# Kernel tuning notes

Hardware: AMD Instinct MI355X
Metric: run time of the kernel (lower is better)

The kernel has to match this reference:

```python
import jax, jax.numpy as jnp
import numpy as np

_SAMPLING_EPS = 1e-5


def setup_inputs() -> dict:
    key = jax.random.key(0)
    k1, k2, k3, k4, k5 = jax.random.split(key, 5)
    B, V = 128, 128000
    logits = jax.random.normal(k1, (B, V), dtype=jnp.float32)
    temperature = jax.random.uniform(k2, (B,), dtype=jnp.float32)
    top_k = jax.random.randint(k3, (B,), 0, 1024)
    top_p = jax.random.uniform(k4, (B,), dtype=jnp.float32)
    # uniform noise -> exponential via -log(u) inside reference (torch's q.exponential_())
    q = jnp.clip(jax.random.uniform(k5, (B, V), dtype=jnp.float32), 1e-10, 1.0)
    return {"logits": logits, "temperature": temperature, "top_k": top_k,
            "top_p": top_p, "q": q, "max_num_logprobs": 5}


def reference(logits, temperature, top_k, top_p, q, max_num_logprobs):
    B, V = logits.shape
    # apply_temperature: temp < eps treated as 1.0 (greedy rows untouched)
    temp = jnp.where(temperature < _SAMPLING_EPS, 1.0, temperature)
    logits = logits.astype(jnp.float32) / temp[:, None]

    # _apply_top_k_top_p: ascending sort over vocab
    idx = jnp.argsort(logits, axis=-1)                      # [B, V]
    ls = jnp.take_along_axis(logits, idx, axis=-1)          # sorted ascending
    k = jnp.clip(top_k.astype(jnp.int32), 1, V)
    thr = jnp.take_along_axis(ls, (V - k)[:, None], axis=-1)  # k-th largest value
    ls = jnp.where(ls < thr, -jnp.inf, ls)
    # top-p on the top-k-masked sorted logits
    ps = jax.nn.softmax(ls, axis=-1)
    cum = jnp.cumsum(ps, axis=-1)
    p_mask = cum <= (1.0 - top_p)[:, None]
    p_mask = p_mask.at[:, -1].set(False)
    ls = jnp.where(p_mask, -jnp.inf, ls)
    # scatter masked sorted logits back to original vocab positions
    rows = jnp.arange(B)[:, None]
    logits = jnp.zeros_like(logits).at[rows, idx].set(ls)

    # get_probs + sample
    probs = jax.nn.softmax(logits, axis=-1)
    e = -jnp.log(q)                                         # exponential noise
    greedy = jnp.argmax(probs, axis=-1)
    rand = jnp.argmax(probs / e, axis=-1)                   # Gumbel-max equivalent
    sampled = jnp.where(temperature < _SAMPLING_EPS, greedy, rand).astype(jnp.int32)

    # top-k logprobs
    logprobs = jax.nn.log_softmax(logits, axis=-1)
    topk_logprobs, topk_indices = jax.lax.top_k(logprobs, max_num_logprobs)
    return sampled, topk_logprobs, topk_indices.astype(jnp.int32)
```

## Files before the change

kernel.cpp:

```cpp
#include <hip/hip_runtime.h>
#include <math.h>
#include <float.h>

typedef unsigned long long u64;
typedef unsigned u32;

#define NT 1024
#define NW 16
#define NT1 256
#define NT4 256
#define SL 8
#define NB 8192
#define BSH 19
#define CAP 2048
#define TOPN 5
#define SCALE_D 17592186044416.0
#define NEG_BIG -3.0e38f

struct RowCtl { u32 kb; u32 cnt0; u32 pad[30]; };

__device__ __forceinline__ u32 key_of(float f){
  u32 u = __float_as_uint(f);
  return (u & 0x80000000u) ? ~u : (u | 0x80000000u);
}
__device__ __forceinline__ float key_to_float(u32 k){
  u32 u = (k & 0x80000000u) ? (k & 0x7FFFFFFFu) : ~k;
  return __uint_as_float(u);
}
__device__ __forceinline__ u64 quantMass(float l, float m){
  float ef = expf(l - m);
  return (u64)((double)ef * SCALE_D + 0.5);
}

struct Top5 { float v[TOPN]; int ix[TOPN]; };
__device__ __forceinline__ void t5_init(Top5& t){
  for (int j=0;j<TOPN;j++){ t.v[j] = -INFINITY; t.ix[j] = 0x7FFFFFFF; }
}
__device__ __forceinline__ void t5_insert(Top5& t, float nv, int ni){
  for (int j=0;j<TOPN;j++){
    if (nv > t.v[j] || (nv == t.v[j] && ni < t.ix[j])){
      for (int s=TOPN-1;s>j;s--){ t.v[s]=t.v[s-1]; t.ix[s]=t.ix[s-1]; }
      t.v[j]=nv; t.ix[j]=ni;
      return;
    }
  }
}

__device__ void scan_excl(u64* arr, int n, u64* wsum){
  const int tid = threadIdx.x, lane = tid & 63, w = tid >> 6;
  __syncthreads();
  const int chunk = (n + NT - 1) / NT;
  const int base = tid * chunk;
  u64 local = 0;
  for (int j=0;j<chunk;j++){ int i=base+j; if (i<n) local += arr[i]; }
  u64 inc = local;
  for (int off=1; off<64; off<<=1){
    u64 up = __shfl_up(inc, off, 64);
    if (lane >= off) inc += up;
  }
  if (lane == 63) wsum[w] = inc;
  __syncthreads();
  if (tid == 0){
    u64 acc = 0;
    for (int i=0;i<NW;i++){ u64 v = wsum[i]; wsum[i] = acc; acc += v; }
    arr[n] = acc;
  }
  __syncthreads();
  u64 run = wsum[w] + (inc - local);
  for (int j=0;j<chunk;j++){ int i=base+j; if (i<n){ u64 v=arr[i]; arr[i]=run; run += v; } }
  __syncthreads();
}

__device__ __forceinline__ void scan_select(u64 (*h)[256], u64 targetIn, bool mkBudget,
        float pB, u32* o_bin, u64* o_excl, u64* o_T, u64* o_budget, int lane){
  const int base = lane*4;
  u64 c0 = h[0][base+0]+h[1][base+0]+h[2][base+0]+h[3][base+0];
  u64 c1 = h[0][base+1]+h[1][base+1]+h[2][base+1]+h[3][base+1];
  u64 c2 = h[0][base+2]+h[1][base+2]+h[2][base+2]+h[3][base+2];
  u64 c3 = h[0][base+3]+h[1][base+3]+h[2][base+3]+h[3][base+3];
  u64 lsum = c0+c1+c2+c3;
  u64 inc = lsum;
  for (int off=1; off<64; off<<=1){
    u64 up = __shfl_up(inc, off, 64);
    if (lane >= off) inc += up;
  }
  u64 total = __shfl(inc, 63, 64);
  u64 target = targetIn;
  if (mkBudget){
    float cf = 1.0f - pB;
    u64 q = (u64)((double)cf * (double)total);
    if (q >= total) q = total - 1;
    target = q;
    if (lane == 0){ *o_T = total; *o_budget = q; }
  }
  u64 run = inc - lsum;
  if (run<=target && target<run+c0){ *o_bin=(u32)base;   *o_excl=run; } run+=c0;
  if (run<=target && target<run+c1){ *o_bin=(u32)base+1; *o_excl=run; } run+=c1;
  if (run<=target && target<run+c2){ *o_bin=(u32)base+2; *o_excl=run; } run+=c2;
  if (run<=target && target<run+c3){ *o_bin=(u32)base+3; *o_excl=run; }
}


__global__ void k0_zero(u32* __restrict__ hist, u32* __restrict__ ctlw, int Bn){
  size_t n = (size_t)Bn * NB;
  size_t stride = (size_t)gridDim.x * blockDim.x;
  for (size_t i = (size_t)blockIdx.x*blockDim.x + threadIdx.x; i < n; i += stride) hist[i] = 0;
  size_t nc = (size_t)Bn * (sizeof(RowCtl)/4);
  for (size_t i = (size_t)blockIdx.x*blockDim.x + threadIdx.x; i < nc; i += stride) ctlw[i] = 0;
}

__global__ __launch_bounds__(NT1) void k1_hist(const float* __restrict__ L,
        const float* __restrict__ temp, u32* __restrict__ hist, int Bn, int Vn){
  __shared__ u32 lh[NB];
  const int b = blockIdx.y, s = blockIdx.x, tid = threadIdx.x;
  for (int j=tid;j<NB;j+=NT1) lh[j]=0;
  const float tr = temp[b]; const float tEff = (tr < 1e-5f) ? 1.0f : tr;
  const float* Lr = L + (size_t)b*Vn;
  const int chunk = (Vn + SL-1)/SL;
  const int i0 = s*chunk, i1 = min(i0+chunk, Vn);
  __syncthreads();
  const int nv = (i1 - i0) / 4;
  const float4* L4 = (const float4*)(Lr + i0);
  for (int v=tid; v<nv; v+=NT1){
    float4 x = L4[v];
    #pragma unroll
    for (int e=0;e<4;e++){
      float l = (&x.x)[e] / tEff;
      atomicAdd(&lh[key_of(l)>>BSH], 1u);
    }
  }
  for (int i=i0+nv*4+tid; i<i1; i+=NT1){
    float l = Lr[i]/tEff;
    atomicAdd(&lh[key_of(l)>>BSH], 1u);
  }
  __syncthreads();
  u32* Hr = hist + (size_t)b*NB;
  for (int j=tid;j<NB;j+=NT1){ u32 c = lh[j]; if (c) atomicAdd(&Hr[j], c); }
}

__global__ __launch_bounds__(NT) void k2_kb(const int* __restrict__ top_k,
        const u32* __restrict__ hist, RowCtl* __restrict__ ctl, int Bn, int Vn){
  __shared__ u32 sh[NB+1];
  __shared__ u32 wsum[NW];
  __shared__ int s_g;
  const int b = blockIdx.x, tid = threadIdx.x, lane = tid&63, w = tid>>6;
  const u32* Hr = hist + (size_t)b*NB;
  for (int j=tid;j<NB;j+=NT) sh[j] = Hr[j];
  __syncthreads();
  const int chunk = NB/NT;
  u32 local=0;
  for (int j=0;j<chunk;j++) local += sh[tid*chunk+j];
  u32 inc = local;
  for (int off=1;off<64;off<<=1){ u32 up=__shfl_up(inc,off,64); if (lane>=off) inc+=up; }
  if (lane==63) wsum[w]=inc;
  __syncthreads();
  if (tid==0){ u32 acc=0; for(int i=0;i<NW;i++){u32 v=wsum[i]; wsum[i]=acc; acc+=v;} sh[NB]=acc; }
  __syncthreads();
  u32 run = wsum[w] + (inc - local);
  for (int j=0;j<chunk;j++){ int i2=tid*chunk+j; u32 v=sh[i2]; sh[i2]=run; run+=v; }
  __syncthreads();
  int kk = top_k[b]; if (kk<1) kk=1; if (kk>Vn) kk=Vn;
  const u32 rank = (u32)(Vn - kk);
  for (int j=tid;j<NB;j+=NT) if (sh[j] <= rank && rank < sh[j+1]) s_g = j;
  __syncthreads();
  if (tid==0) ctl[b].kb = (u32)s_g;
}

__global__ __launch_bounds__(NT1) void k3_collect(const float* __restrict__ L,
        const float* __restrict__ temp, u64* __restrict__ cand, RowCtl* __restrict__ ctl,
        int Bn, int Vn){
  const int b = blockIdx.y, s = blockIdx.x, tid = threadIdx.x;
  const float tr = temp[b]; const float tEff = (tr<1e-5f)?1.0f:tr;
  const u32 kbMinKey = ctl[b].kb << BSH;
  const float* Lr = L + (size_t)b*Vn;
  u64* Cr = cand + (size_t)b*CAP;
  const int chunk = (Vn + SL-1)/SL;
  const int i0 = s*chunk, i1 = min(i0+chunk, Vn);
  const int nv = (i1 - i0) / 4;
  const float4* L4 = (const float4*)(Lr + i0);
  const int lane = tid & 63;
  for (int v=tid; v<nv; v+=NT1){
    float4 x = L4[v];
    #pragma unroll
    for (int e=0;e<4;e++){
      float l = (&x.x)[e] / tEff;
      u32 k = key_of(l);
      bool pred = (k >= kbMinKey);
      u64 mk = __ballot(pred);
      if (mk){
        int leader = __ffsll((long long)mk) - 1;
        u32 base = 0;
        if (lane == leader) base = atomicAdd(&ctl[b].cnt0, (u32)__popcll(mk));
        base = __shfl(base, leader, 64);
        if (pred){
          u32 p = base + (u32)__popcll(mk & ((1ull<<lane)-1ull));
          if (p < CAP) Cr[p] = ((u64)k<<32) | (u64)(u32)(i0 + v*4 + e);
        }
      }
    }
  }
  for (int i=i0+nv*4+tid; i<i1; i+=NT1){
    float l = Lr[i]/tEff;
    u32 k = key_of(l);
    if (k >= kbMinKey){
      u32 p = atomicAdd(&ctl[b].cnt0, 1u);
      if (p < CAP) Cr[p] = ((u64)k<<32) | (u64)(u32)i;
    }
  }
}

__global__ __launch_bounds__(NT4) void k4_solve(const float* __restrict__ L,
        const float* __restrict__ temp, const int* __restrict__ top_k,
        const float* __restrict__ top_p, const float* __restrict__ qn,
        const u64* __restrict__ cand, const RowCtl* __restrict__ ctl,
        float* __restrict__ out, int Bn, int Vn){
  __shared__ u32 sk[CAP];
  __shared__ u32 si[CAP];
  __shared__ u64 sm_[CAP];
  __shared__ u64 h[4][256];
  __shared__ u32 s_mk;
  __shared__ u32 s_bin;
  __shared__ u64 s_excl;
  __shared__ u64 s_T;
  __shared__ u64 s_budget;
  __shared__ float s_fill[16];
  __shared__ Top5 s_wt5[NT4/64];
  __shared__ double s_wr[NT4/64];
  __shared__ int s_wri[NT4/64];
  __shared__ int s_wg[NT4/64];

  const int b = blockIdx.x, tid = threadIdx.x, lane = tid&63, w = tid>>6;
  const u32 n0raw = ctl[b].cnt0;
  if (n0raw == 0 || n0raw > CAP) return;
  const int n0 = (int)n0raw;
  const float tr = temp[b]; const float tEff = (tr<1e-5f)?1.0f:tr;
  const float* Lr = L + (size_t)b*Vn;
  const float* Qr = qn + (size_t)b*Vn;
  const u64* Cr = cand + (size_t)b*CAP;

  if (tid==0) s_mk = 0;
  __syncthreads();
  u32 mk = 0;
  for (int p=tid; p<n0; p+=NT4){
    u64 e = Cr[p];
    u32 k = (u32)(e>>32);
    sk[p] = k; si[p] = (u32)e;
    mk = max(mk, k);
  }
  for (int off=32; off; off>>=1){ u32 o = __shfl_xor(mk, off, 64); mk = max(mk, o); }
  if (lane==0) atomicMax(&s_mk, mk);
  if (tid<16) s_fill[tid] = (tid<Vn) ? Lr[tid] : 0.f;
  __syncthreads();
  const u32 mKey = s_mk;
  const float m = key_to_float(mKey);

  int kk = top_k[b]; if (kk<1) kk=1; if (kk>Vn) kk=Vn; if (kk>n0) kk=n0;
  u64 rA = (u64)(n0 - kk);
  u32 pfx=0, pmask=0;
  for (int lev=0; lev<4; lev++){
    const int sh = 24 - 8*lev;
    for (int j=tid;j<1024;j+=NT4) ((u64*)h)[j] = 0;
    __syncthreads();
    for (int p=tid;p<n0;p+=NT4){
      u32 k = sk[p];
      if ((k & pmask) == pfx) atomicAdd(&h[w][(k>>sh)&0xFFu], 1ull);
    }
    __syncthreads();
    if (w==0) scan_select(h, rA, false, 0.f, &s_bin, &s_excl, 0, 0, lane);
    __syncthreads();
    pfx |= (s_bin << sh); pmask |= (0xFFu << sh);
    rA -= s_excl;
  }
  const u32 thrKey = pfx;

  for (int p=tid;p<n0;p+=NT4)
    sm_[p] = (sk[p] >= thrKey) ? quantMass(key_to_float(sk[p]), m) : 0ull;
  const float pB = top_p[b];

  u32 pfx2=0, pmask2=0;
  u64 Qloc=0, maskedBelow=0;
  for (int lev=0; lev<4; lev++){
    const int sh = 24 - 8*lev;
    for (int j=tid;j<1024;j+=NT4) ((u64*)h)[j] = 0;
    __syncthreads();
    for (int p=tid;p<n0;p+=NT4){
      u64 ms = sm_[p];
      if (ms && ((sk[p] & pmask2) == pfx2)) atomicAdd(&h[w][(sk[p]>>sh)&0xFFu], ms);
    }
    __syncthreads();
    if (w==0) scan_select(h, Qloc, lev==0, pB, &s_bin, &s_excl, &s_T, &s_budget, lane);
    __syncthreads();
    if (lev==0) Qloc = s_budget;
    pfx2 |= (s_bin << sh); pmask2 |= (0xFFu << sh);
    maskedBelow += s_excl;
    Qloc -= s_excl;
  }
  const u32 vKey = pfx2;
  const u64 T = s_T;
  const u64 qstar = quantMass(key_to_float(vKey), m);
  u64 tmask = qstar ? (Qloc / qstar) : 0ull;

  int idxStar = -1;
  if (tmask > 0){
    u64 r2 = tmask - 1;
    u32 ipfx=0, imask=0;
    for (int lev=0; lev<4; lev++){
      const int sh = 24 - 8*lev;
      for (int j=tid;j<1024;j+=NT4) ((u64*)h)[j] = 0;
      __syncthreads();
      for (int p=tid;p<n0;p+=NT4){
        if (sk[p]==vKey && ((si[p] & imask) == ipfx))
          atomicAdd(&h[w][(si[p]>>sh)&0xFFu], 1ull);
      }
      __syncthreads();
      if (w==0) scan_select(h, r2, false, 0.f, &s_bin, &s_excl, 0, 0, lane);
      __syncthreads();
      ipfx |= (s_bin << sh); imask |= (0xFFu << sh);
      r2 -= s_excl;
    }
    idxStar = (int)ipfx;
  }
  const u64 S2 = T - maskedBelow - tmask*qstar;

  Top5 t5; t5_init(t5);
  double br = -1.0; int bri = 0x7FFFFFFF; int gmin = 0x7FFFFFFF;
  for (int p=tid; p<n0; p+=NT4){
    u32 k = sk[p]; int idx = (int)si[p];
    bool surv = (k > vKey) || (k == vKey && idx > idxStar);
    if (surv){
      float l = key_to_float(k);
      float u = expf(l - m);
      float e = -logf(Qr[idx]);
      double ratio = (double)u / (double)e;
      if (ratio > br || (ratio == br && idx < bri)){ br = ratio; bri = idx; }
      if (k == mKey && idx < gmin) gmin = idx;
      t5_insert(t5, l, idx);
    }
  }
  for (int off=1; off<64; off<<=1){
    Top5 o;
    for (int j=0;j<TOPN;j++){ o.v[j]=__shfl_xor(t5.v[j],off,64); o.ix[j]=__shfl_xor(t5.ix[j],off,64); }
    for (int j=0;j<TOPN;j++) t5_insert(t5, o.v[j], o.ix[j]);
    double orr = __shfl_xor(br, off, 64); int ori = __shfl_xor(bri, off, 64);
    if (orr > br || (orr == br && ori < bri)){ br = orr; bri = ori; }
    int og = __shfl_xor(gmin, off, 64); if (og < gmin) gmin = og;
  }
  if (lane==0){ s_wt5[w]=t5; s_wr[w]=br; s_wri[w]=bri; s_wg[w]=gmin; }
  __syncthreads();
  if (tid==0){
    Top5 f = s_wt5[0];
    double fr = s_wr[0]; int fri = s_wri[0]; int fg = s_wg[0];
    for (int wi=1; wi<NT4/64; wi++){
      for (int j=0;j<TOPN;j++) t5_insert(f, s_wt5[wi].v[j], s_wt5[wi].ix[j]);
      if (s_wr[wi] > fr || (s_wr[wi]==fr && s_wri[wi]<fri)){ fr=s_wr[wi]; fri=s_wri[wi]; }
      if (s_wg[wi] < fg) fg = s_wg[wi];
    }
    int filled = 0;
    for (int i=0; i<16 && i<Vn && filled<TOPN; i++){
      u32 k2 = key_of(s_fill[i]/tEff);
      bool surv2 = (k2 > vKey) || (k2 == vKey && i > idxStar);
      if (!surv2){ t5_insert(f, -INFINITY, i); filled++; }
    }
    double lS = log((double)S2 / SCALE_D);
    int sampled = (tr < 1e-5f) ? fg : fri;
    out[b] = (float)sampled;
    for (int j=0;j<TOPN;j++){
      float lv = f.v[j];
      float lp = (lv == -INFINITY) ? NEG_BIG : (float)((double)lv - (double)m - lS);
      out[Bn + b*TOPN + j] = lp;
      out[Bn + Bn*TOPN + b*TOPN + j] = (float)f.ix[j];
    }
  }
}


__device__ void find_cross(const u64* arr, int n, u64 target, int* s_fh, u64* s_fb){
  const int tid = threadIdx.x;
  const int chunk = (n + NT - 1) / NT;
  const int base = tid * chunk;
  for (int j=0;j<chunk;j++){
    int i = base + j;
    if (i < n && arr[i] <= target && target < arr[i+1]){ *s_fh = i; *s_fb = arr[i]; }
  }
  __syncthreads();
}

__device__ void fallback_row(int b, const float* logits, const float* temperature,
                             const int* top_k, const float* top_p, const float* qnoise,
                             float* out, int Bn, int Vn){
  __shared__ u64 s_hist[4097];
  __shared__ u64 s_wsum[NW];
  __shared__ int s_fh;
  __shared__ u64 s_fb;
  __shared__ float s_fm[NW];
  __shared__ float s_m;
  __shared__ int s_lastMax;
  __shared__ int s_eqcnt;
  __shared__ int s_eqlist[1024];
  __shared__ int s_sel;
  __shared__ Top5 s_wt5[NW];
  __shared__ double s_wr[NW];
  __shared__ int s_wri[NW];
  __shared__ int s_wg[NW];
  __shared__ u64 s_ws2[NW];

  const int tid = threadIdx.x, lane = tid & 63, w = tid >> 6;
  const float* L  = logits + (size_t)b * Vn;
  const float* Qr = qnoise + (size_t)b * Vn;
  const float tRaw = temperature[b];
  const float tEff = (tRaw < 1e-5f) ? 1.0f : tRaw;

  for (int i=tid;i<4097;i+=NT) s_hist[i] = 0;
  if (tid==0){ s_lastMax = -1; s_eqcnt = 0; }
  __syncthreads();
  float lm = -INFINITY;
  for (int i=tid;i<Vn;i+=NT){
    float l = L[i] / tEff;
    u32 k = key_of(l);
    atomicAdd(&s_hist[k>>20], 1ull);
    lm = fmaxf(lm, l);
  }
  for (int off=32; off; off>>=1) lm = fmaxf(lm, __shfl_xor(lm, off, 64));
  if (lane==0) s_fm[w] = lm;
  scan_excl(s_hist, 4096, s_wsum);
  if (tid==0){ float mm=-INFINITY; for (int i=0;i<NW;i++) mm=fmaxf(mm,s_fm[i]); s_m=mm; }
  __syncthreads();
  const float m = s_m;

  int kk = top_k[b]; if (kk < 1) kk = 1; if (kk > Vn) kk = Vn;
  u64 r = (u64)(Vn - kk);
  find_cross(s_hist, 4096, r, &s_fh, &s_fb);
  const int kb0 = s_fh; r -= s_fb;
  __syncthreads();

  for (int i=tid;i<4097;i+=NT) s_hist[i]=0;
  __syncthreads();
  for (int i=tid;i<Vn;i+=NT){
    float l = L[i]/tEff; u32 k = key_of(l);
    if ((int)(k>>20) == kb0) atomicAdd(&s_hist[(k>>8)&0xFFFu], 1ull);
  }
  scan_excl(s_hist, 4096, s_wsum);
  find_cross(s_hist, 4096, r, &s_fh, &s_fb);
  const int kb1 = s_fh; r -= s_fb;
  __syncthreads();

  const u32 ktop24 = ((u32)kb0<<12) | (u32)kb1;
  for (int i=tid;i<4097;i+=NT) s_hist[i]=0;
  __syncthreads();
  for (int i=tid;i<Vn;i+=NT){
    float l = L[i]/tEff; u32 k = key_of(l);
    if ((k>>8) == ktop24) atomicAdd(&s_hist[k & 0xFFu], 1ull);
  }
  scan_excl(s_hist, 256, s_wsum);
  find_cross(s_hist, 256, r, &s_fh, &s_fb);
  const u32 thrKey = (ktop24<<8) | (u32)s_fh;
  const float thr = key_to_float(thrKey);
  __syncthreads();

  for (int i=tid;i<4097;i+=NT) s_hist[i]=0;
  __syncthreads();
  for (int i=tid;i<Vn;i+=NT){
    float l = L[i]/tEff;
    if (l >= thr){
      u32 k = key_of(l);
      double sd = exp((double)l - (double)m);
      u64 qv = (u64)(sd * SCALE_D + 0.5);
      atomicAdd(&s_hist[k>>20], qv);
      if (l == m) atomicMax(&s_lastMax, i);
    }
  }
  scan_excl(s_hist, 4096, s_wsum);
  const u64 T = s_hist[4096];
  const float cf = 1.0f - top_p[b];
  const double qtd = (double)cf * (double)T;
  u64 Qfix = (qtd >= (double)T) ? T : (u64)qtd;
  const bool allmask = (Qfix >= T);

  u32 vKey = 0xFFFFFFFFu;
  int idxStar = 0x7FFFFFFF;

  if (!allmask){
    find_cross(s_hist, 4096, Qfix, &s_fh, &s_fb);
    const int g0 = s_fh;
    u64 Qrem = Qfix - s_fb;
    __syncthreads();

    for (int i=tid;i<4097;i+=NT) s_hist[i]=0;
    __syncthreads();
    for (int i=tid;i<Vn;i+=NT){
      float l = L[i]/tEff;
      if (l >= thr){
        u32 k = key_of(l);
        if ((int)(k>>20) == g0){
          double sd = exp((double)l - (double)m);
          atomicAdd(&s_hist[(k>>8)&0xFFFu], (u64)(sd*SCALE_D+0.5));
        }
      }
    }
    scan_excl(s_hist, 4096, s_wsum);
    find_cross(s_hist, 4096, Qrem, &s_fh, &s_fb);
    const int g1 = s_fh; Qrem -= s_fb;
    __syncthreads();

    const u32 ptop24 = ((u32)g0<<12)|(u32)g1;
    for (int i=tid;i<4097;i+=NT) s_hist[i]=0;
    __syncthreads();
    for (int i=tid;i<Vn;i+=NT){
      float l = L[i]/tEff;
      if (l >= thr){
        u32 k = key_of(l);
        if ((k>>8) == ptop24){
          double sd = exp((double)l - (double)m);
          atomicAdd(&s_hist[k & 0xFFu], (u64)(sd*SCALE_D+0.5));
        }
      }
    }
    scan_excl(s_hist, 256, s_wsum);
    find_cross(s_hist, 256, Qrem, &s_fh, &s_fb);
    const int g2 = s_fh;
    const u64 base2 = s_fb;
    const u64 nextPref = s_hist[g2+1];
    Qrem -= base2;
    vKey = (ptop24<<8) | (u32)g2;
    const float vStar = key_to_float(vKey);
    const double sv = exp((double)vStar - (double)m);
    const u64 qstar = (u64)(sv*SCALE_D+0.5);
    u64 nstar = (qstar > 0) ? (nextPref - base2) / qstar : 1ull;
    if (nstar < 1) nstar = 1;
    u64 tmask = (qstar > 0) ? (Qrem / qstar) : 0ull;
    if (tmask >= nstar) tmask = nstar - 1;
    idxStar = -1;
    __syncthreads();
    if (tmask >= 1){
      for (int i=tid;i<Vn;i+=NT){
        float l = L[i]/tEff;
        if (key_of(l) == vKey){
          int p = atomicAdd(&s_eqcnt, 1);
          if (p < 1024) s_eqlist[p] = i;
        }
      }
      __syncthreads();
      if (tid == 0){
        int n_ = s_eqcnt; if (n_ > 1024) n_ = 1024;
        for (int a=1;a<n_;a++){
          int key0 = s_eqlist[a]; int c2=a-1;
          while (c2>=0 && s_eqlist[c2]>key0){ s_eqlist[c2+1]=s_eqlist[c2]; c2--; }
          s_eqlist[c2+1]=key0;
        }
        int ti = (int)tmask - 1;
        if (ti >= n_) ti = n_-1;
        s_sel = s_eqlist[ti];
      }
      __syncthreads();
      idxStar = s_sel;
    }
  }

  const int lastMax = s_lastMax;
  Top5 t5; t5_init(t5);
  u64 s2 = 0;
  double br = -1.0; int bri = 0x7FFFFFFF;
  int gmin = 0x7FFFFFFF;
  for (int i=tid;i<Vn;i+=NT){
    float l = L[i]/tEff;
    u32 k = key_of(l);
    bool surv = (l >= thr) &&
                ((k > vKey) || (k == vKey && i > idxStar) || (i == lastMax));
    float val;
    if (surv){
      double sd = exp((double)l - (double)m);
      s2 += (u64)(sd*SCALE_D+0.5);
      float u = expf(l - m);
      float e = -logf(Qr[i]);
      double ratio = (double)u / (double)e;
      if (ratio > br || (ratio == br && i < bri)){ br = ratio; bri = i; }
      if (l == m && i < gmin) gmin = i;
      val = l;
    } else {
      val = -INFINITY;
    }
    t5_insert(t5, val, i);
  }
  for (int off=1; off<64; off<<=1){
    Top5 o;
    for (int j=0;j<TOPN;j++){ o.v[j]=__shfl_xor(t5.v[j],off,64); o.ix[j]=__shfl_xor(t5.ix[j],off,64); }
    for (int j=0;j<TOPN;j++) t5_insert(t5, o.v[j], o.ix[j]);
    double orr = __shfl_xor(br, off, 64);
    int ori = __shfl_xor(bri, off, 64);
    if (orr > br || (orr == br && ori < bri)){ br = orr; bri = ori; }
    int og = __shfl_xor(gmin, off, 64); if (og < gmin) gmin = og;
    s2 += __shfl_xor(s2, off, 64);
  }
  if (lane == 0){
    s_wt5[w] = t5; s_wr[w]=br; s_wri[w]=bri; s_wg[w]=gmin; s_ws2[w]=s2;
  }
  __syncthreads();
  if (tid == 0){
    Top5 f = s_wt5[0];
    double fr = s_wr[0]; int fri = s_wri[0]; int fg = s_wg[0];
    u64 fs2 = s_ws2[0];
    for (int wi=1; wi<NW; wi++){
      for (int j=0;j<TOPN;j++) t5_insert(f, s_wt5[wi].v[j], s_wt5[wi].ix[j]);
      if (s_wr[wi] > fr || (s_wr[wi]==fr && s_wri[wi]<fri)){ fr=s_wr[wi]; fri=s_wri[wi]; }
      if (s_wg[wi] < fg) fg = s_wg[wi];
      fs2 += s_ws2[wi];
    }
    double S2d = (double)fs2 / SCALE_D;
    double lS = log(S2d);
    int sampled = (tRaw < 1e-5f) ? fg : fri;
    out[b] = (float)sampled;
    for (int j=0;j<TOPN;j++){
      float lv = f.v[j];
      float lp = (lv == -INFINITY) ? NEG_BIG : (float)((double)lv - (double)m - lS);
      out[Bn + b*TOPN + j] = lp;
      out[Bn + Bn*TOPN + b*TOPN + j] = (float)f.ix[j];
    }
  }
}

__global__ __launch_bounds__(NT) void k5_rowfb(const float* __restrict__ logits,
        const float* __restrict__ temperature, const int* __restrict__ top_k,
        const float* __restrict__ top_p, const float* __restrict__ qnoise,
        const RowCtl* __restrict__ ctl, float* __restrict__ out, int Bn, int Vn){
  const int b = blockIdx.x;
  const u32 c = ctl[b].cnt0;
  if (c > 0 && c <= CAP) return;
  fallback_row(b, logits, temperature, top_k, top_p, qnoise, out, Bn, Vn);
}

extern "C" __global__ void __launch_bounds__(NT)
sampler_fallback(const float* __restrict__ logits, const float* __restrict__ temperature,
                 const int* __restrict__ top_k, const float* __restrict__ top_p,
                 const float* __restrict__ qnoise, float* __restrict__ out, int Bn, int Vn){
  fallback_row(blockIdx.x, logits, temperature, top_k, top_p, qnoise, out, Bn, Vn);
}


extern "C" void kernel_launch(void* const* d_in, const int* in_sizes, int n_in,
                              void* d_out, int out_size, void* d_ws, size_t ws_size,
                              hipStream_t stream)
{
  const float* logits      = (const float*)d_in[0];
  const float* temperature = (const float*)d_in[1];
  const int*   top_k       = (const int*)d_in[2];
  const float* top_p       = (const float*)d_in[3];
  const float* q           = (const float*)d_in[4];
  const int Bn = in_sizes[1];
  const int Vn = in_sizes[0] / Bn;

  const size_t offCand = (size_t)Bn * NB * 4;
  const size_t offCtl  = offCand + (size_t)Bn * CAP * 8;
  const size_t total   = offCtl + (size_t)Bn * sizeof(RowCtl);

  if (ws_size < total){
    sampler_fallback<<<dim3(Bn), dim3(NT), 0, stream>>>(
        logits, temperature, top_k, top_p, q, (float*)d_out, Bn, Vn);
    return;
  }

  char* wsb = (char*)d_ws;
  u32*    hist = (u32*)wsb;
  u64*    cand = (u64*)(wsb + offCand);
  RowCtl* ctl  = (RowCtl*)(wsb + offCtl);

  k0_zero   <<<dim3(512),     dim3(256), 0, stream>>>(hist, (u32*)ctl, Bn);
  k1_hist   <<<dim3(SL, Bn),  dim3(NT1), 0, stream>>>(logits, temperature, hist, Bn, Vn);
  k2_kb     <<<dim3(Bn),      dim3(NT),  0, stream>>>(top_k, hist, ctl, Bn, Vn);
  k3_collect<<<dim3(SL, Bn),  dim3(NT1), 0, stream>>>(logits, temperature, cand, ctl, Bn, Vn);
  k4_solve  <<<dim3(Bn),      dim3(NT4), 0, stream>>>(logits, temperature, top_k, top_p, q,
                                                      cand, ctl, (float*)d_out, Bn, Vn);
  k5_rowfb  <<<dim3(Bn),      dim3(NT),  0, stream>>>(logits, temperature, top_k, top_p, q,
                                                      ctl, (float*)d_out, Bn, Vn);
}
```

Measured before the change: 139.7 us.

## Replace radix-histogram selection in solve kernel with register-resident bitwise radix select

The solve kernel now keeps each thread's candidate keys and indices in registers (8 per thread) instead of shared-memory arrays. The three 4-pass, 8-bit shared histogram selections (top-k threshold, top-p mass cutoff, tie index) become bit-by-bit binary searches using wave reductions and a small double-buffered shared slot. Searches start at the highest bit where the candidate floor and the max key differ. This removes the histogram clears, shared atomics and scan passes, at the cost of one barrier per bit and more iterations overall.

```diff
diff --git a/kernel.cpp b/kernel.cpp
--- a/kernel.cpp
+++ b/kernel.cpp
@@ -9,6 +9,7 @@
 #define NW 16
 #define NT1 256
 #define NT4 256
+#define EPT 8
 #define SL 8
 #define NB 8192
 #define BSH 19
@@ -69,35 +70,6 @@
   u64 run = wsum[w] + (inc - local);
   for (int j=0;j<chunk;j++){ int i=base+j; if (i<n){ u64 v=arr[i]; arr[i]=run; run += v; } }
   __syncthreads();
-}
-
-__device__ __forceinline__ void scan_select(u64 (*h)[256], u64 targetIn, bool mkBudget,
-        float pB, u32* o_bin, u64* o_excl, u64* o_T, u64* o_budget, int lane){
-  const int base = lane*4;
-  u64 c0 = h[0][base+0]+h[1][base+0]+h[2][base+0]+h[3][base+0];
-  u64 c1 = h[0][base+1]+h[1][base+1]+h[2][base+1]+h[3][base+1];
-  u64 c2 = h[0][base+2]+h[1][base+2]+h[2][base+2]+h[3][base+2];
-  u64 c3 = h[0][base+3]+h[1][base+3]+h[2][base+3]+h[3][base+3];
-  u64 lsum = c0+c1+c2+c3;
-  u64 inc = lsum;
-  for (int off=1; off<64; off<<=1){
-    u64 up = __shfl_up(inc, off, 64);
-    if (lane >= off) inc += up;
-  }
-  u64 total = __shfl(inc, 63, 64);
-  u64 target = targetIn;
-  if (mkBudget){
-    float cf = 1.0f - pB;
-    u64 q = (u64)((double)cf * (double)total);
-    if (q >= total) q = total - 1;
-    target = q;
-    if (lane == 0){ *o_T = total; *o_budget = q; }
-  }
-  u64 run = inc - lsum;
-  if (run<=target && target<run+c0){ *o_bin=(u32)base;   *o_excl=run; } run+=c0;
-  if (run<=target && target<run+c1){ *o_bin=(u32)base+1; *o_excl=run; } run+=c1;
-  if (run<=target && target<run+c2){ *o_bin=(u32)base+2; *o_excl=run; } run+=c2;
-  if (run<=target && target<run+c3){ *o_bin=(u32)base+3; *o_excl=run; }
 }
 
 
@@ -214,15 +186,8 @@
         const float* __restrict__ top_p, const float* __restrict__ qn,
         const u64* __restrict__ cand, const RowCtl* __restrict__ ctl,
         float* __restrict__ out, int Bn, int Vn){
-  __shared__ u32 sk[CAP];
-  __shared__ u32 si[CAP];
-  __shared__ u64 sm_[CAP];
-  __shared__ u64 h[4][256];
+  __shared__ u64 s_red[2][4];
   __shared__ u32 s_mk;
-  __shared__ u32 s_bin;
-  __shared__ u64 s_excl;
-  __shared__ u64 s_T;
-  __shared__ u64 s_budget;
   __shared__ float s_fill[16];
   __shared__ Top5 s_wt5[NT4/64];
   __shared__ double s_wr[NT4/64];
@@ -237,103 +202,156 @@
   const float* Lr = L + (size_t)b*Vn;
   const float* Qr = qn + (size_t)b*Vn;
   const u64* Cr = cand + (size_t)b*CAP;
+  const u32 kbMinKey = ctl[b].kb << BSH;
 
   if (tid==0) s_mk = 0;
-  __syncthreads();
+  if (tid<16) s_fill[tid] = (tid<Vn) ? Lr[tid] : 0.f;
+  __syncthreads();
+  u32 k_[EPT], ix_[EPT];
+  u32 valid = 0;
   u32 mk = 0;
-  for (int p=tid; p<n0; p+=NT4){
-    u64 e = Cr[p];
-    u32 k = (u32)(e>>32);
-    sk[p] = k; si[p] = (u32)e;
-    mk = max(mk, k);
-  }
-  for (int off=32; off; off>>=1){ u32 o = __shfl_xor(mk, off, 64); mk = max(mk, o); }
+  #pragma unroll
+  for (int e=0;e<EPT;e++){
+    int p = tid + e*NT4;
+    if (p < n0){
+      u64 v = Cr[p];
+      k_[e] = (u32)(v>>32); ix_[e] = (u32)v;
+      valid |= 1u<<e;
+      mk = max(mk, k_[e]);
+    } else { k_[e]=0u; ix_[e]=0u; }
+  }
+  for (int off=32; off; off>>=1){ u32 o=__shfl_xor(mk,off,64); mk=max(mk,o); }
   if (lane==0) atomicMax(&s_mk, mk);
-  if (tid<16) s_fill[tid] = (tid<Vn) ? Lr[tid] : 0.f;
   __syncthreads();
   const u32 mKey = s_mk;
   const float m = key_to_float(mKey);
+  int buf = 0;
 
   int kk = top_k[b]; if (kk<1) kk=1; if (kk>Vn) kk=Vn; if (kk>n0) kk=n0;
-  u64 rA = (u64)(n0 - kk);
-  u32 pfx=0, pmask=0;
-  for (int lev=0; lev<4; lev++){
-    const int sh = 24 - 8*lev;
-    for (int j=tid;j<1024;j+=NT4) ((u64*)h)[j] = 0;
+  u32 rA = (u32)(n0 - kk);
+  const u32 xA = kbMinKey ^ mKey;
+  const int sbA = xA ? (31 - __clz(xA)) : -1;
+  u32 pfx = (sbA==31) ? 0u : (mKey & ((sbA>=0) ? ~((1u<<(sbA+1))-1u) : 0xFFFFFFFFu));
+  u32 aA = valid;
+  for (int bit=sbA; bit>=0; --bit){
+    u32 c0 = 0;
+    #pragma unroll
+    for (int e=0;e<EPT;e++)
+      c0 += ((aA>>e)&1u) & (((k_[e]>>bit)&1u)^1u);
+    for (int off=32; off; off>>=1) c0 += __shfl_xor(c0, off, 64);
+    if (lane==0) s_red[buf][w] = (u64)c0;
     __syncthreads();
-    for (int p=tid;p<n0;p+=NT4){
-      u32 k = sk[p];
-      if ((k & pmask) == pfx) atomicAdd(&h[w][(k>>sh)&0xFFu], 1ull);
-    }
+    u32 C0 = (u32)(s_red[buf][0]+s_red[buf][1]+s_red[buf][2]+s_red[buf][3]);
+    u32 chosen;
+    if (rA < C0) chosen = 0u;
+    else { rA -= C0; chosen = 1u; pfx |= (1u<<bit); }
+    u32 na = 0;
+    #pragma unroll
+    for (int e=0;e<EPT;e++)
+      na |= (((aA>>e)&1u) & ((((k_[e]>>bit)&1u)==chosen)?1u:0u)) << e;
+    aA = na;
+    buf ^= 1;
+  }
+  const u32 thrKey = pfx;
+
+  u64 ms_[EPT];
+  u32 aB = 0;
+  u64 locT = 0;
+  #pragma unroll
+  for (int e=0;e<EPT;e++){
+    bool sv = ((valid>>e)&1u) && (k_[e] >= thrKey);
+    ms_[e] = sv ? quantMass(key_to_float(k_[e]), m) : 0ull;
+    if (sv) aB |= 1u<<e;
+    locT += ms_[e];
+  }
+  for (int off=32; off; off>>=1) locT += __shfl_xor(locT, off, 64);
+  if (lane==0) s_red[buf][w] = locT;
+  __syncthreads();
+  const u64 T = s_red[buf][0]+s_red[buf][1]+s_red[buf][2]+s_red[buf][3];
+  buf ^= 1;
+  const float cf = 1.0f - top_p[b];
+  u64 Q = (u64)((double)cf * (double)T);
+  if (Q >= T) Q = T - 1;
+  const u64 budget = Q;
+
+  const u32 xB = thrKey ^ mKey;
+  const int sbB = xB ? (31 - __clz(xB)) : -1;
+  u32 pfx2 = (sbB==31) ? 0u : (mKey & ((sbB>=0) ? ~((1u<<(sbB+1))-1u) : 0xFFFFFFFFu));
+  for (int bit=sbB; bit>=0; --bit){
+    u64 S0 = 0;
+    #pragma unroll
+    for (int e=0;e<EPT;e++)
+      if (((aB>>e)&1u) && !((k_[e]>>bit)&1u)) S0 += ms_[e];
+    for (int off=32; off; off>>=1) S0 += __shfl_xor(S0, off, 64);
+    if (lane==0) s_red[buf][w] = S0;
     __syncthreads();
-    if (w==0) scan_select(h, rA, false, 0.f, &s_bin, &s_excl, 0, 0, lane);
-    __syncthreads();
-    pfx |= (s_bin << sh); pmask |= (0xFFu << sh);
-    rA -= s_excl;
-  }
-  const u32 thrKey = pfx;
-
-  for (int p=tid;p<n0;p+=NT4)
-    sm_[p] = (sk[p] >= thrKey) ? quantMass(key_to_float(sk[p]), m) : 0ull;
-  const float pB = top_p[b];
-
-  u32 pfx2=0, pmask2=0;
-  u64 Qloc=0, maskedBelow=0;
-  for (int lev=0; lev<4; lev++){
-    const int sh = 24 - 8*lev;
-    for (int j=tid;j<1024;j+=NT4) ((u64*)h)[j] = 0;
-    __syncthreads();
-    for (int p=tid;p<n0;p+=NT4){
-      u64 ms = sm_[p];
-      if (ms && ((sk[p] & pmask2) == pfx2)) atomicAdd(&h[w][(sk[p]>>sh)&0xFFu], ms);
-    }
-    __syncthreads();
-    if (w==0) scan_select(h, Qloc, lev==0, pB, &s_bin, &s_excl, &s_T, &s_budget, lane);
-    __syncthreads();
-    if (lev==0) Qloc = s_budget;
-    pfx2 |= (s_bin << sh); pmask2 |= (0xFFu << sh);
-    maskedBelow += s_excl;
-    Qloc -= s_excl;
+    u64 St = s_red[buf][0]+s_red[buf][1]+s_red[buf][2]+s_red[buf][3];
+    u32 chosen;
+    if (Q < St) chosen = 0u;
+    else { Q -= St; chosen = 1u; pfx2 |= (1u<<bit); }
+    u32 na = 0;
+    #pragma unroll
+    for (int e=0;e<EPT;e++)
+      na |= (((aB>>e)&1u) & ((((k_[e]>>bit)&1u)==chosen)?1u:0u)) << e;
+    aB = na;
+    buf ^= 1;
   }
   const u32 vKey = pfx2;
-  const u64 T = s_T;
   const u64 qstar = quantMass(key_to_float(vKey), m);
-  u64 tmask = qstar ? (Qloc / qstar) : 0ull;
+  const u64 tmask = qstar ? (Q / qstar) : 0ull;
+  const u64 S2 = T - (budget - Q) - tmask*qstar;
 
   int idxStar = -1;
   if (tmask > 0){
-    u64 r2 = tmask - 1;
-    u32 ipfx=0, imask=0;
-    for (int lev=0; lev<4; lev++){
-      const int sh = 24 - 8*lev;
-      for (int j=tid;j<1024;j+=NT4) ((u64*)h)[j] = 0;
+    u32 r2 = (u32)(tmask - 1);
+    u32 aC = 0;
+    #pragma unroll
+    for (int e=0;e<EPT;e++)
+      if (((valid>>e)&1u) && k_[e]==vKey) aC |= 1u<<e;
+    const int sbC = 31 - __clz((u32)(Vn-1));
+    u32 pfx3 = 0;
+    for (int bit=sbC; bit>=0; --bit){
+      u32 c0 = 0;
+      #pragma unroll
+      for (int e=0;e<EPT;e++)
+        c0 += ((aC>>e)&1u) & (((ix_[e]>>bit)&1u)^1u);
+      for (int off=32; off; off>>=1) c0 += __shfl_xor(c0, off, 64);
+      if (lane==0) s_red[buf][w] = (u64)c0;
       __syncthreads();
-      for (int p=tid;p<n0;p+=NT4){
-        if (sk[p]==vKey && ((si[p] & imask) == ipfx))
-          atomicAdd(&h[w][(si[p]>>sh)&0xFFu], 1ull);
-      }
-      __syncthreads();
-      if (w==0) scan_select(h, r2, false, 0.f, &s_bin, &s_excl, 0, 0, lane);
-      __syncthreads();
-      ipfx |= (s_bin << sh); imask |= (0xFFu << sh);
-      r2 -= s_excl;
-    }
-    idxStar = (int)ipfx;
-  }
-  const u64 S2 = T - maskedBelow - tmask*qstar;
-
+      u32 C0 = (u32)(s_red[buf][0]+s_red[buf][1]+s_red[buf][2]+s_red[buf][3]);
+      u32 chosen;
+      if (r2 < C0) chosen = 0u;
+      else { r2 -= C0; chosen = 1u; pfx3 |= (1u<<bit); }
+      u32 na = 0;
+      #pragma unroll
+      for (int e=0;e<EPT;e++)
+        na |= (((aC>>e)&1u) & ((((ix_[e]>>bit)&1u)==chosen)?1u:0u)) << e;
+      aC = na;
+      buf ^= 1;
+    }
+    idxStar = (int)pfx3;
+  }
+
+  u32 sv = 0;
+  float qv[EPT];
+  #pragma unroll
+  for (int e=0;e<EPT;e++){
+    bool s = ((valid>>e)&1u) &&
+             ((k_[e] > vKey) || (k_[e] == vKey && (int)ix_[e] > idxStar));
+    if (s) sv |= 1u<<e;
+    qv[e] = s ? Qr[ix_[e]] : 1.0f;
+  }
   Top5 t5; t5_init(t5);
   double br = -1.0; int bri = 0x7FFFFFFF; int gmin = 0x7FFFFFFF;
-  for (int p=tid; p<n0; p+=NT4){
-    u32 k = sk[p]; int idx = (int)si[p];
-    bool surv = (k > vKey) || (k == vKey && idx > idxStar);
-    if (surv){
-      float l = key_to_float(k);
+  #pragma unroll
+  for (int e=0;e<EPT;e++){
+    if ((sv>>e)&1u){
+      float l = key_to_float(k_[e]); int idx = (int)ix_[e];
       float u = expf(l - m);
-      float e = -logf(Qr[idx]);
-      double ratio = (double)u / (double)e;
+      float ee = -logf(qv[e]);
+      double ratio = (double)u / (double)ee;
       if (ratio > br || (ratio == br && idx < bri)){ br = ratio; bri = idx; }
-      if (k == mKey && idx < gmin) gmin = idx;
+      if (k_[e] == mKey && idx < gmin) gmin = idx;
       t5_insert(t5, l, idx);
     }
   }
```

New measurement: 156.2 us. +11.8%, slower.
